# Performance work log

Hardware: AMD Instinct MI355X
Metric: run time of the kernel (lower is better)

The kernel has to match this reference:

```python
import jax, jax.numpy as jnp
import numpy as np

B, L, H, V = 64, 8, 4096, 50257


def setup_inputs() -> dict:
    key = jax.random.key(0)
    ks = jax.random.split(key, 5)
    return {
        "embedding": jax.random.normal(ks[0], (V, H), jnp.float32) * 0.02,
        "hidden_states": jax.random.normal(ks[1], (B, L, H), jnp.float32),
        "output_position": 7,  # scalar index of the position to sample from
        "temperatures": jax.random.uniform(ks[2], (B,), jnp.float32, 0.5, 1.5),
        "top_ps": jax.random.uniform(ks[3], (B,), jnp.float32, 0.7, 1.0),
        "tops_ks": jax.random.randint(ks[4], (B,), 1, 64),  # top-k in [1,64)
        "embedding_bias": jnp.zeros((V,), jnp.float32),
    }


def reference(embedding, hidden_states, output_position, temperatures, top_ps, tops_ks, embedding_bias):
    # select the output position: [B, H]
    h = hidden_states[:, output_position, :]
    # logits GEMM against tied embedding: [B, V]
    logits = jnp.einsum("bh,vh->bv", h, embedding) + embedding_bias[None, :]
    logits = logits / temperatures[:, None]
    probs = jax.nn.softmax(logits.astype(jnp.float32), axis=-1)

    # descending sort of probabilities
    order = jnp.argsort(-probs, axis=-1)                       # [B, V]
    probs_sort = jnp.take_along_axis(probs, order, axis=-1)    # [B, V]

    # top-p mask: exclusive cumulative sum exceeding top_p
    cum = jnp.cumsum(probs_sort, axis=-1)
    topp_mask = (cum - probs_sort) > top_ps[:, None]
    # top-k mask: rank >= k
    ranks = jnp.arange(V, dtype=tops_ks.dtype)[None, :]
    topk_mask = ranks >= tops_ks[:, None]

    probs_sort = jnp.where(topp_mask | topk_mask, 0.0, probs_sort)
    probs_sort = probs_sort / jnp.sum(probs_sort, axis=-1, keepdims=True)

    # scatter back to original vocab order via inverse permutation
    inv = jnp.argsort(order, axis=-1)
    probs_final = jnp.take_along_axis(probs_sort, inv, axis=-1)  # [B, V]

    # multinomial sampling (1 sample per row)
    logp = jnp.where(probs_final > 0, jnp.log(jnp.maximum(probs_final, 1e-38)), -jnp.inf)
    next_token_ids = jax.random.categorical(jax.random.key(42), logp, axis=-1)
    return next_token_ids
```

## Files before the change

kernel.cpp:

```cpp
#include <hip/hip_runtime.h>
#include <stdint.h>
#include <float.h>
#include <limits.h>


typedef __bf16 bf16x8 __attribute__((ext_vector_type(8)));
typedef float  f32x4  __attribute__((ext_vector_type(4)));

__device__ __forceinline__ void split8v(const float* f, bf16x8& hi, bf16x8& lo) {
#pragma unroll
    for (int e = 0; e < 8; ++e) {
        const __bf16 h = (__bf16)f[e];
        hi[e] = h;
        lo[e] = (__bf16)(f[e] - (float)h);
    }
}
__device__ __forceinline__ void split8(const float* f, uint4& hi, uint4& lo) {
    bf16x8 vh, vl;
    split8v(f, vh, vl);
    hi = __builtin_bit_cast(uint4, vh);
    lo = __builtin_bit_cast(uint4, vl);
}

__global__ __launch_bounds__(256) void prep_h(
    const float* __restrict__ hs, const int* __restrict__ pos_p,
    unsigned short* __restrict__ Ahi, unsigned short* __restrict__ Alo,
    int H, int L)
{
    const int pos = pos_p[0];
    const int tid = blockIdx.x * 256 + threadIdx.x;
    const int b     = tid >> 8;
    const int kbase = (tid & 255) * 16;
    const float* src = hs + ((size_t)b * L + pos) * H + kbase;
    float f[16];
    *(float4*)&f[0]  = *(const float4*)(src);
    *(float4*)&f[4]  = *(const float4*)(src + 4);
    *(float4*)&f[8]  = *(const float4*)(src + 8);
    *(float4*)&f[12] = *(const float4*)(src + 12);

    const int r16 = b >> 4, ll = b & 15;
    const int kc  = kbase >> 5;
    const int lh0 = (kbase >> 3) & 3;
#pragma unroll
    for (int c = 0; c < 2; ++c) {
        uint4 hi, lo;
        split8(f + 8 * c, hi, lo);
        const size_t dst = ((size_t)(r16 * (H >> 5) + kc) * 64 + (lh0 + c) * 16 + ll) * 8;
        *(uint4*)&Ahi[dst] = hi;
        *(uint4*)&Alo[dst] = lo;
    }
}

#define NWF 256

__global__ __launch_bounds__(256, 5) void logits_mfma(
    const float* __restrict__ emb,
    const unsigned short* __restrict__ Ahi,
    const unsigned short* __restrict__ Alo,
    const float* __restrict__ temps,
    const float* __restrict__ bias,
    float*       __restrict__ out,
    int V, int H)
{
    __shared__ float sB[2][16 * NWF];

    const int tid  = threadIdx.x;
    const int lane = tid & 63;
    const int w    = tid >> 6;
    const int v0   = blockIdx.x * 16;

    const int ll  = lane & 15;
    const int lh  = lane >> 4;
    const int swz = ll << 2;

    const int NW = H / NWF;

    const unsigned short* pAh = Ahi + (size_t)w * ((size_t)H * 16)
                              + (size_t)lh * 128 + (size_t)ll * 8;
    const unsigned short* pAl = Alo + (size_t)w * ((size_t)H * 16)
                              + (size_t)lh * 128 + (size_t)ll * 8;

    f32x4 acc = (f32x4){0.f, 0.f, 0.f, 0.f};

#define STAGE(win, slot) do {                                                 \
    _Pragma("unroll")                                                         \
    for (int rr = 0; rr < 4; ++rr) {                                          \
        const int r = w * 4 + rr;                                             \
        int rg = v0 + r;                                                      \
        rg = (rg < V) ? rg : (V - 1);                                         \
        const float* srcp = emb + (size_t)rg * H + (size_t)(win) * NWF        \
                          + ((lane * 4) ^ ((r & 15) << 2));                   \
        __builtin_amdgcn_global_load_lds(                                     \
            (const __attribute__((address_space(1))) void*)srcp,              \
            (__attribute__((address_space(3))) void*)&sB[slot][r * NWF],      \
            16, 0, 0);                                                        \
    }                                                                         \
} while (0)

    STAGE(0, 0);
    __syncthreads();

    for (int win = 0; win < NW; ++win) {
        const int bf = win & 1;
        if (win + 1 < NW) STAGE(win + 1, bf ^ 1);

        const size_t tbase = (size_t)win * 8;
#pragma unroll
        for (int kt = 0; kt < 8; ++kt) {
            const size_t ai = (tbase + kt) * 512;
            const bf16x8 ah = *(const bf16x8*)&pAh[ai];
            const bf16x8 al = *(const bf16x8*)&pAl[ai];

            const int f0 = kt * 32 + lh * 8;
            float f[8];
            *(float4*)&f[0] = *(const float4*)&sB[bf][ll * NWF + ((f0)     ^ swz)];
            *(float4*)&f[4] = *(const float4*)&sB[bf][ll * NWF + ((f0 + 4) ^ swz)];
            bf16x8 fbh, fbl;
            split8v(f, fbh, fbl);

            acc = __builtin_amdgcn_mfma_f32_16x16x32_bf16(al, fbh, acc, 0, 0, 0);
            acc = __builtin_amdgcn_mfma_f32_16x16x32_bf16(ah, fbl, acc, 0, 0, 0);
            acc = __builtin_amdgcn_mfma_f32_16x16x32_bf16(ah, fbh, acc, 0, 0, 0);
        }
        __syncthreads();
    }
#undef STAGE

    const int vv = v0 + ll;
    if (vv < V) {
        const float bv = bias[vv];
#pragma unroll
        for (int r = 0; r < 4; ++r) {
            const int b = w * 16 + lh * 4 + r;
            out[(size_t)b * V + vv] = (acc[r] + bv) / temps[b];
        }
    }
}

__device__ __forceinline__ uint32_t rotl32(uint32_t x, int d) {
    return (x << d) | (x >> (32 - d));
}

__device__ float jax_gumbel(uint32_t flat) {
    const uint32_t k0 = 0u, k1 = 42u;
    const uint32_t ks[3] = { k0, k1, k0 ^ k1 ^ 0x1BD11BDAu };
    uint32_t x0 = 0u   + ks[0];
    uint32_t x1 = flat + ks[1];
    const int rot[2][4] = { {13, 15, 26, 6}, {17, 29, 16, 24} };
#pragma unroll
    for (int r = 0; r < 5; ++r) {
        const int* rr = rot[r & 1];
#pragma unroll
        for (int j = 0; j < 4; ++j) {
            x0 += x1;
            x1 = rotl32(x1, rr[j]);
            x1 ^= x0;
        }
        x0 += ks[(r + 1) % 3];
        x1 += ks[(r + 2) % 3] + (uint32_t)(r + 1);
    }
    const uint32_t bits = x0 ^ x1;
    const uint32_t fb = (bits >> 9) | 0x3F800000u;
    const float f = __uint_as_float(fb) - 1.0f;
    const float tiny = 1.17549435e-38f;
    float u = __fadd_rn(__fmul_rn(f, 1.0f), tiny);
    u = fmaxf(tiny, u);
    const float l1 = logf(u);
    return -logf(-l1);
}

#define NBINS 4096
#define CAP   2048
#define NKEEP 64

__global__ __launch_bounds__(256) void sample_kernel(
    const float* __restrict__ logits,
    const float* __restrict__ top_ps,
    const int*   __restrict__ top_ks,
    int*         __restrict__ out_ids,
    int V)
{
    const int b = blockIdx.x;
    const int tid = threadIdx.x;
    const float* row = logits + (size_t)b * V;

    __shared__ float swred[4];
    __shared__ int   bins[NBINS];
    __shared__ int   schunk[256];
    __shared__ int   sThrBin, sCnt, sMkeep;
    __shared__ float cval[CAP];
    __shared__ int   cidx[CAP];
    __shared__ float tval[NKEEP];
    __shared__ int   tidxs[NKEEP];

    float m = -INFINITY;
    for (int k = tid; k < V; k += 256) m = fmaxf(m, row[k]);
#pragma unroll
    for (int o = 32; o > 0; o >>= 1) m = fmaxf(m, __shfl_xor(m, o, 64));
    if ((tid & 63) == 0) swred[tid >> 6] = m;
    __syncthreads();
    m = fmaxf(fmaxf(swred[0], swred[1]), fmaxf(swred[2], swred[3]));

    for (int k = tid; k < NBINS; k += 256) bins[k] = 0;
    if (tid == 0) sCnt = 0;
    __syncthreads();

    float s = 0.f;
    for (int k = tid; k < V; k += 256) {
        const float x = row[k];
        s += expf(x - m);
        const float g = m - x;
        int bin = (int)(g * 256.0f);
        if (bin >= NBINS) bin = NBINS - 1;
        atomicAdd(&bins[bin], 1);
    }
#pragma unroll
    for (int o = 32; o > 0; o >>= 1) s += __shfl_xor(s, o, 64);
    __syncthreads();
    if ((tid & 63) == 0) swred[tid >> 6] = s;

    int csum = 0;
#pragma unroll
    for (int k = 0; k < NBINS / 256; ++k) csum += bins[tid * (NBINS / 256) + k];
    schunk[tid] = csum;
    __syncthreads();
    s = swred[0] + swred[1] + swred[2] + swred[3];
    if (tid == 0) {
        int cum = 0, chunk = 255;
        for (int c = 0; c < 256; ++c) {
            if (cum + schunk[c] >= NKEEP) { chunk = c; break; }
            cum += schunk[c];
        }
        int t = NBINS - 1;
        const int base = chunk * (NBINS / 256);
        for (int k = base; k < base + NBINS / 256; ++k) {
            cum += bins[k];
            if (cum >= NKEEP) { t = k; break; }
        }
        sThrBin = t;
    }
    __syncthreads();
    const int thrBin = sThrBin;

    for (int k = tid; k < V; k += 256) {
        const float x = row[k];
        const float g = m - x;
        int bin = (int)(g * 256.0f);
        if (bin >= NBINS) bin = NBINS - 1;
        if (bin <= thrBin) {
            const int p = atomicAdd(&sCnt, 1);
            if (p < CAP) { cval[p] = x; cidx[p] = k; }
        }
    }
    __syncthreads();
    const int C = min(sCnt, CAP);

    for (int i = tid; i < C; i += 256) {
        const float vi = cval[i];
        const int   ii = cidx[i];
        int rank = 0;
        for (int j = 0; j < C; ++j) {
            const float vj = cval[j];
            const int   ij = cidx[j];
            rank += (vj > vi) || (vj == vi && ij < ii);
        }
        if (rank < NKEEP) { tval[rank] = vi; tidxs[rank] = ii; }
    }
    __syncthreads();

    if (tid == 0) {
        const float pb = top_ps[b];
        const int   kk = top_ks[b];
        const int   nk = min(NKEEP, C);
        float cum = 0.f;
        int mk = 0;
        for (int r = 0; r < nk; ++r) {
            const float pr = expf(tval[r] - m) / s;
            cum += pr;
            const float excl = cum - pr;
            if (excl > pb || r >= kk) break;
            ++mk;
        }
        sMkeep = (mk > 0) ? mk : 1;
    }
    __syncthreads();
    const int mkeep = sMkeep;

    if (tid < 64) {
        float sc = -INFINITY;
        int vid = INT_MAX;
        if (tid < mkeep) {
            const int v = tidxs[tid];
            vid = v;
            sc = tval[tid] + jax_gumbel((uint32_t)b * (uint32_t)V + (uint32_t)v);
        }
#pragma unroll
        for (int o = 32; o > 0; o >>= 1) {
            const float os = __shfl_xor(sc, o, 64);
            const int   ov = __shfl_xor(vid, o, 64);
            if (os > sc || (os == sc && ov < vid)) { sc = os; vid = ov; }
        }
        if (tid == 0) out_ids[b] = vid;
    }
}

extern "C" void kernel_launch(void* const* d_in, const int* in_sizes, int n_in,
                              void* d_out, int out_size, void* d_ws, size_t ws_size,
                              hipStream_t stream)
{
    const float* emb   = (const float*)d_in[0];
    const float* hs    = (const float*)d_in[1];
    const int*   pos   = (const int*)d_in[2];
    const float* temps = (const float*)d_in[3];
    const float* tps   = (const float*)d_in[4];
    const int*   tks   = (const int*)d_in[5];
    const float* bias  = (const float*)d_in[6];

    const int B = in_sizes[3];
    const int V = in_sizes[6];
    const int H = (int)((long long)in_sizes[0] / V);
    const int L = (int)((long long)in_sizes[1] / ((long long)B * H));

    float*          logits = (float*)d_ws;
    unsigned short* Ahi    = (unsigned short*)((char*)d_ws + (16u << 20));
    unsigned short* Alo    = Ahi + (size_t)B * H;

    prep_h<<<(B * H) / (16 * 256), 256, 0, stream>>>(hs, pos, Ahi, Alo, H, L);

    const int nblk = (V + 15) / 16;
    logits_mfma<<<nblk, 256, 0, stream>>>(emb, Ahi, Alo, temps, bias,
                                          logits, V, H);

    sample_kernel<<<B, 256, 0, stream>>>(logits, tps, tks, (int*)d_out, V);
}
```

Baseline: 370.4 us.

## Stage embedding tiles through registers and batch-prefetch A fragments per window

```diff
diff --git a/kernel.cpp b/kernel.cpp
--- a/kernel.cpp
+++ b/kernel.cpp
@@ -53,7 +53,7 @@
 
 #define NWF 256
 
-__global__ __launch_bounds__(256, 5) void logits_mfma(
+__global__ __launch_bounds__(256, 4) void logits_mfma(
     const float* __restrict__ emb,
     const unsigned short* __restrict__ Ahi,
     const unsigned short* __restrict__ Alo,
@@ -80,37 +80,52 @@
     const unsigned short* pAl = Alo + (size_t)w * ((size_t)H * 16)
                               + (size_t)lh * 128 + (size_t)ll * 8;
 
-    f32x4 acc = (f32x4){0.f, 0.f, 0.f, 0.f};
-
-#define STAGE(win, slot) do {                                                 \
+    const float* bsrc[4];
+#pragma unroll
+    for (int rr = 0; rr < 4; ++rr) {
+        int rg = v0 + w * 4 + rr;
+        rg = (rg < V) ? rg : (V - 1);
+        bsrc[rr] = emb + (size_t)rg * H + lane * 4;
+    }
+
+    float4 pf[4];
+    bf16x8 awh[8], awl[8];
+    f32x4  acc = (f32x4){0.f, 0.f, 0.f, 0.f};
+
+#define LOADB(win) do {                                                       \
+    _Pragma("unroll")                                                         \
+    for (int rr = 0; rr < 4; ++rr)                                            \
+        pf[rr] = *(const float4*)(bsrc[rr] + (size_t)(win) * NWF);            \
+} while (0)
+
+#define WRITEB(slot) do {                                                     \
     _Pragma("unroll")                                                         \
     for (int rr = 0; rr < 4; ++rr) {                                          \
         const int r = w * 4 + rr;                                             \
-        int rg = v0 + r;                                                      \
-        rg = (rg < V) ? rg : (V - 1);                                         \
-        const float* srcp = emb + (size_t)rg * H + (size_t)(win) * NWF        \
-                          + ((lane * 4) ^ ((r & 15) << 2));                   \
-        __builtin_amdgcn_global_load_lds(                                     \
-            (const __attribute__((address_space(1))) void*)srcp,              \
-            (__attribute__((address_space(3))) void*)&sB[slot][r * NWF],      \
-            16, 0, 0);                                                        \
+        *(float4*)&sB[slot][r * NWF + ((lane * 4) ^ ((r & 15) << 2))] = pf[rr]; \
     }                                                                         \
 } while (0)
 
-    STAGE(0, 0);
+#define LOADA(win) do {                                                       \
+    _Pragma("unroll")                                                         \
+    for (int kt = 0; kt < 8; ++kt) {                                          \
+        const size_t ai = ((size_t)(win) * 8 + kt) * 512;                     \
+        awh[kt] = *(const bf16x8*)&pAh[ai];                                   \
+        awl[kt] = *(const bf16x8*)&pAl[ai];                                   \
+    }                                                                         \
+} while (0)
+
+    LOADB(0);
+    WRITEB(0);
     __syncthreads();
 
     for (int win = 0; win < NW; ++win) {
         const int bf = win & 1;
-        if (win + 1 < NW) STAGE(win + 1, bf ^ 1);
-
-        const size_t tbase = (size_t)win * 8;
+        LOADA(win);
+        if (win + 1 < NW) LOADB(win + 1);
+
 #pragma unroll
         for (int kt = 0; kt < 8; ++kt) {
-            const size_t ai = (tbase + kt) * 512;
-            const bf16x8 ah = *(const bf16x8*)&pAh[ai];
-            const bf16x8 al = *(const bf16x8*)&pAl[ai];
-
             const int f0 = kt * 32 + lh * 8;
             float f[8];
             *(float4*)&f[0] = *(const float4*)&sB[bf][ll * NWF + ((f0)     ^ swz)];
@@ -118,13 +133,16 @@
             bf16x8 fbh, fbl;
             split8v(f, fbh, fbl);
 
-            acc = __builtin_amdgcn_mfma_f32_16x16x32_bf16(al, fbh, acc, 0, 0, 0);
-            acc = __builtin_amdgcn_mfma_f32_16x16x32_bf16(ah, fbl, acc, 0, 0, 0);
-            acc = __builtin_amdgcn_mfma_f32_16x16x32_bf16(ah, fbh, acc, 0, 0, 0);
-        }
+            acc = __builtin_amdgcn_mfma_f32_16x16x32_bf16(awl[kt], fbh, acc, 0, 0, 0);
+            acc = __builtin_amdgcn_mfma_f32_16x16x32_bf16(awh[kt], fbl, acc, 0, 0, 0);
+            acc = __builtin_amdgcn_mfma_f32_16x16x32_bf16(awh[kt], fbh, acc, 0, 0, 0);
+        }
+        if (win + 1 < NW) WRITEB(bf ^ 1);
         __syncthreads();
     }
-#undef STAGE
+#undef LOADB
+#undef WRITEB
+#undef LOADA
 
     const int vv = v0 + ll;
     if (vv < V) {
```

After: 603.6 us. 63.0% more time.
